# Kernel optimization log

Measured on AMD Instinct MI355X. Metric: run time of the kernel, lower is better.

The kernel has to match this reference:

```python
import jax, jax.numpy as jnp
import numpy as np

K = 3          # kernel_size
P = K // 2     # padding


def setup_inputs() -> dict:
    key = jax.random.key(0)
    # [B, C, H, W]; first C-4 channels are per-class probabilities, last 4 are box offsets
    points = jax.random.normal(key, (4, 84, 512, 512), dtype=jnp.float32)
    return {"points": points}


def reference(points):
    # Peak (point) NMS: keep a pixel iff torch.argmax over its KxK window of
    # max-class-probability lands exactly on the window center.
    # torch.argmax returns the FIRST flat index attaining the max, so the center
    # survives iff it is strictly greater than every earlier (row-major) window
    # element and >= every later element.
    probs = jnp.max(points[:, :-4], axis=1)            # [B, H, W]
    B, H, W = probs.shape
    padded = jnp.pad(probs, ((0, 0), (P, P), (P, P)))  # zero pad, matches F.pad default
    center_idx = P * K + P
    mask = jnp.ones((B, H, W), dtype=bool)
    for di in range(K):                                # small fixed K*K loop (8 iters)
        for dj in range(K):
            idx = di * K + dj
            if idx == center_idx:
                continue
            nb = padded[:, di:di + H, dj:dj + W]       # neighbor value at this offset
            cmp = (probs > nb) if idx < center_idx else (probs >= nb)
            mask = mask & cmp
    # non-peaks zeroed across ALL channels, exactly like the zeros_like + scatter
    return points * mask[:, None, :, :].astype(points.dtype)
```

## Files before the change

### kernel.cpp

```cpp
#include <hip/hip_runtime.h>

#define BB 4
#define CC 84
#define CM 80
#define HH 512
#define WW 512
#define HWSZ (HH * WW)
#define PG (HWSZ / 4)
#define NCH 4
#define CPC (CM / NCH)

typedef float v4f __attribute__((ext_vector_type(4)));

static __device__ __forceinline__ v4f vmax4(v4f a, v4f b) {
    v4f r;
    r.x = fmaxf(a.x, b.x);
    r.y = fmaxf(a.y, b.y);
    r.z = fmaxf(a.z, b.z);
    r.w = fmaxf(a.w, b.w);
    return r;
}

__global__ __launch_bounds__(256) void partial_max_kernel(const float* __restrict__ pts,
                                                          float* __restrict__ partial) {
    int tid = blockIdx.x * blockDim.x + threadIdx.x;
    int pg  = tid & (PG - 1);
    int r   = tid >> 16;
    int chunk = r % NCH;
    int b     = r / NCH;

    const v4f* base = (const v4f*)pts + ((size_t)b * CC + chunk * CPC) * PG + pg;
    v4f m = __builtin_nontemporal_load(base);
#pragma unroll 5
    for (int c = 1; c < CPC; ++c) {
        v4f v = __builtin_nontemporal_load(base + (size_t)c * PG);
        m = vmax4(m, v);
    }
    ((v4f*)partial)[((size_t)chunk * BB + b) * PG + pg] = m;
}

__global__ __launch_bounds__(256) void fused_mask_kernel(const float* __restrict__ partial,
                                                         float* __restrict__ mask) {
    int tid = blockIdx.x * blockDim.x + threadIdx.x;
    int pg  = tid & (PG - 1);
    int b   = tid >> 16;
    int off = pg << 2;
    int h   = off >> 9;
    int w0  = off & (WW - 1);

    float rows[3][6];
#pragma unroll
    for (int r = 0; r < 3; ++r) {
        int hh = h + r - 1;
        bool hv = (hh >= 0) & (hh < HH);
#pragma unroll
        for (int ci = 0; ci < 6; ++ci) {
            int ww = w0 + ci - 1;
            bool wv = (ww >= 0) & (ww < WW);
            float v = 0.0f;
            if (hv & wv) {
                int pidx = hh * WW + ww;
                v = partial[(size_t)(0 * BB + b) * HWSZ + pidx];
#pragma unroll
                for (int ch = 1; ch < NCH; ++ch)
                    v = fmaxf(v, partial[(size_t)(ch * BB + b) * HWSZ + pidx]);
            }
            rows[r][ci] = v;
        }
    }

    v4f fm;
#pragma unroll
    for (int j = 0; j < 4; ++j) {
        float v = rows[1][j + 1];
        bool m = (v >  rows[0][j]) & (v >  rows[0][j + 1]) & (v >  rows[0][j + 2])
               & (v >  rows[1][j]) & (v >= rows[1][j + 2])
               & (v >= rows[2][j]) & (v >= rows[2][j + 1]) & (v >= rows[2][j + 2]);
        float f = m ? 1.0f : 0.0f;
        if (j == 0) fm.x = f;
        else if (j == 1) fm.y = f;
        else if (j == 2) fm.z = f;
        else fm.w = f;
    }
    ((v4f*)mask)[(size_t)b * PG + pg] = fm;
}

__global__ __launch_bounds__(256) void mul_kernel(const float* __restrict__ pts,
                                                  const float* __restrict__ mask,
                                                  float* __restrict__ out) {
    int gid = blockIdx.x;
    int c   = gid % CC;
    int pc  = gid / CC;
    int b   = pc >> 8;
    int pg  = ((pc & 255) << 8) + threadIdx.x;

    v4f m = ((const v4f*)mask)[(size_t)b * PG + pg];
    size_t idx = ((size_t)b * CC + c) * PG + pg;

    unsigned nz = (__float_as_uint(m.x) | __float_as_uint(m.y) |
                   __float_as_uint(m.z) | __float_as_uint(m.w));
    v4f o;
    if (nz) {
        v4f v = __builtin_nontemporal_load((const v4f*)pts + idx);
        o.x = v.x * m.x;
        o.y = v.y * m.y;
        o.z = v.z * m.z;
        o.w = v.w * m.w;
    } else {
        o.x = 0.f; o.y = 0.f; o.z = 0.f; o.w = 0.f;
    }
    __builtin_nontemporal_store(o, (v4f*)out + idx);
}

__global__ __launch_bounds__(256) void probs_kernel_fb(const float* __restrict__ pts,
                                                       float* __restrict__ probs) {
    int tid = blockIdx.x * blockDim.x + threadIdx.x;
    int pix = tid << 2;
    int b   = pix >> 18;
    int off = pix & (HWSZ - 1);
    const float4* base = (const float4*)(pts + (size_t)b * CC * HWSZ + off);
    float4 m = base[0];
#pragma unroll 4
    for (int c = 1; c < CM; ++c) {
        float4 v = base[c * (HWSZ / 4)];
        m.x = fmaxf(m.x, v.x); m.y = fmaxf(m.y, v.y);
        m.z = fmaxf(m.z, v.z); m.w = fmaxf(m.w, v.w);
    }
    ((float4*)probs)[tid] = m;
}

__global__ __launch_bounds__(256) void nms_mul_kernel_fb(const float* __restrict__ pts,
                                                         const float* __restrict__ probs,
                                                         float* __restrict__ out) {
    int tid = blockIdx.x * blockDim.x + threadIdx.x;
    int pix = tid << 2;
    int b   = pix >> 18;
    int off = pix & (HWSZ - 1);
    int h   = off >> 9;
    int w0  = off & (WW - 1);
    const float* pb = probs + b * HWSZ;
    float rows[3][6];
#pragma unroll
    for (int r = 0; r < 3; ++r) {
        int hh = h + r - 1;
        bool hv = (hh >= 0) & (hh < HH);
        const float* rp = pb + hh * WW;
#pragma unroll
        for (int ci = 0; ci < 6; ++ci) {
            int ww = w0 + ci - 1;
            bool wv = (ww >= 0) & (ww < WW);
            rows[r][ci] = (hv & wv) ? rp[ww] : 0.0f;
        }
    }
    float fm[4];
    bool any = false;
#pragma unroll
    for (int j = 0; j < 4; ++j) {
        float v = rows[1][j + 1];
        bool m = (v >  rows[0][j]) & (v >  rows[0][j + 1]) & (v >  rows[0][j + 2])
               & (v >  rows[1][j]) & (v >= rows[1][j + 2])
               & (v >= rows[2][j]) & (v >= rows[2][j + 1]) & (v >= rows[2][j + 2]);
        fm[j] = m ? 1.0f : 0.0f;
        any |= m;
    }
    size_t bo = (size_t)b * CC * HWSZ + off;
    const float4* src = (const float4*)(pts + bo);
    float4* dst = (float4*)(out + bo);
    if (any) {
#pragma unroll 4
        for (int c = 0; c < CC; ++c) {
            float4 v = src[c * (HWSZ / 4)];
            float4 o;
            o.x = v.x * fm[0]; o.y = v.y * fm[1];
            o.z = v.z * fm[2]; o.w = v.w * fm[3];
            dst[c * (HWSZ / 4)] = o;
        }
    } else {
        float4 z = make_float4(0.f, 0.f, 0.f, 0.f);
#pragma unroll 4
        for (int c = 0; c < CC; ++c) dst[c * (HWSZ / 4)] = z;
    }
}

extern "C" void kernel_launch(void* const* d_in, const int* in_sizes, int n_in,
                              void* d_out, int out_size, void* d_ws, size_t ws_size,
                              hipStream_t stream) {
    const float* pts = (const float*)d_in[0];
    float* out = (float*)d_out;
    float* ws  = (float*)d_ws;

    const size_t MB4 = (size_t)BB * HWSZ * sizeof(float);
    dim3 blk(256);
    dim3 grd_pg(BB * PG / 256);

    if (ws_size >= (NCH + 1) * MB4) {
        float* partial = ws;
        float* mask    = ws + (size_t)NCH * BB * HWSZ;
        partial_max_kernel<<<dim3(BB * NCH * PG / 256), blk, 0, stream>>>(pts, partial);
        fused_mask_kernel<<<grd_pg, blk, 0, stream>>>(partial, mask);
        mul_kernel<<<dim3(BB * CC * (PG / 256)), blk, 0, stream>>>(pts, mask, out);
    } else {
        float* probs = ws;
        probs_kernel_fb<<<grd_pg, blk, 0, stream>>>(pts, probs);
        nms_mul_kernel_fb<<<grd_pg, blk, 0, stream>>>(pts, probs, out);
    }
}
```

Before: 613.8 us.

## Fuse max, mask and multiply stages into one cooperative grid-synced kernel

Replaces the three-launch pipeline with a single cooperative kernel that runs channel-max, 3x3 peak mask and masked multiply as grid-stride phases separated by grid syncs. The channel max is split into two 40-channel chunks instead of four, shrinking the partial buffer, and the multiply phase processes 42 channels per thread. First-pass loads are made regular (cacheable) rather than nontemporal, possibly letting the large last-level cache serve part of the second read of the input. Risks are grid-sync cost, lower memory-level parallelism per phase, and launch failure falling back to the old path.

```diff
diff --git a/kernel.cpp b/kernel.cpp
--- a/kernel.cpp
+++ b/kernel.cpp
@@ -1,4 +1,7 @@
 #include <hip/hip_runtime.h>
+#include <hip/hip_cooperative_groups.h>
+
+namespace cg = cooperative_groups;
 
 #define BB 4
 #define CC 84
@@ -7,8 +10,6 @@
 #define WW 512
 #define HWSZ (HH * WW)
 #define PG (HWSZ / 4)
-#define NCH 4
-#define CPC (CM / NCH)
 
 typedef float v4f __attribute__((ext_vector_type(4)));
 
@@ -21,6 +22,102 @@
     return r;
 }
 
+__global__ __launch_bounds__(256, 8) void fused_coop(const float* __restrict__ pts,
+                                                     float* __restrict__ wsp,
+                                                     float* __restrict__ out) {
+    float* partial = wsp;
+    float* mask    = wsp + (size_t)2 * BB * HWSZ;
+    const int nth  = gridDim.x * 256;
+    const int tid0 = blockIdx.x * 256 + threadIdx.x;
+
+    for (int t = tid0; t < BB * 2 * PG; t += nth) {
+        int pg    = t & (PG - 1);
+        int r     = t >> 16;
+        int b     = r & 3;
+        int chunk = r >> 2;
+        const v4f* base = (const v4f*)pts + ((size_t)b * CC + chunk * 40) * PG + pg;
+        v4f m = base[0];
+#pragma unroll 8
+        for (int c = 1; c < 40; ++c)
+            m = vmax4(m, base[(size_t)c * PG]);
+        ((v4f*)partial)[((size_t)chunk * BB + b) * PG + pg] = m;
+    }
+    cg::this_grid().sync();
+
+    for (int t = tid0; t < BB * PG; t += nth) {
+        int pg  = t & (PG - 1);
+        int b   = t >> 16;
+        int off = pg << 2;
+        int h   = off >> 9;
+        int w0  = off & (WW - 1);
+
+        const float* p0 = partial + (size_t)b * HWSZ;
+        const float* p1 = partial + (size_t)(BB + b) * HWSZ;
+
+        float rows[3][6];
+#pragma unroll
+        for (int rr = 0; rr < 3; ++rr) {
+            int hh = h + rr - 1;
+            bool hv = (hh >= 0) & (hh < HH);
+#pragma unroll
+            for (int ci = 0; ci < 6; ++ci) {
+                int ww = w0 + ci - 1;
+                bool wv = (ww >= 0) & (ww < WW);
+                float v = 0.0f;
+                if (hv & wv) {
+                    int pidx = hh * WW + ww;
+                    v = fmaxf(p0[pidx], p1[pidx]);
+                }
+                rows[rr][ci] = v;
+            }
+        }
+
+        v4f fm;
+#pragma unroll
+        for (int j = 0; j < 4; ++j) {
+            float v = rows[1][j + 1];
+            bool m = (v >  rows[0][j]) & (v >  rows[0][j + 1]) & (v >  rows[0][j + 2])
+                   & (v >  rows[1][j]) & (v >= rows[1][j + 2])
+                   & (v >= rows[2][j]) & (v >= rows[2][j + 1]) & (v >= rows[2][j + 2]);
+            float f = m ? 1.0f : 0.0f;
+            if (j == 0) fm.x = f;
+            else if (j == 1) fm.y = f;
+            else if (j == 2) fm.z = f;
+            else fm.w = f;
+        }
+        ((v4f*)mask)[(size_t)b * PG + pg] = fm;
+    }
+    cg::this_grid().sync();
+
+    for (int t = tid0; t < BB * 2 * PG; t += nth) {
+        int pg   = t & (PG - 1);
+        int r    = t >> 16;
+        int b    = r >> 1;
+        int half = r & 1;
+        v4f m = ((const v4f*)mask)[(size_t)b * PG + pg];
+        unsigned nz = (__float_as_uint(m.x) | __float_as_uint(m.y) |
+                       __float_as_uint(m.z) | __float_as_uint(m.w));
+        size_t base = ((size_t)b * CC + half * 42) * PG + pg;
+        if (nz) {
+#pragma unroll 7
+            for (int j = 0; j < 42; ++j) {
+                v4f v = __builtin_nontemporal_load((const v4f*)pts + base + (size_t)j * PG);
+                v4f o = v * m;
+                __builtin_nontemporal_store(o, (v4f*)out + base + (size_t)j * PG);
+            }
+        } else {
+            v4f z;
+            z.x = 0.f; z.y = 0.f; z.z = 0.f; z.w = 0.f;
+#pragma unroll 7
+            for (int j = 0; j < 42; ++j)
+                __builtin_nontemporal_store(z, (v4f*)out + base + (size_t)j * PG);
+        }
+    }
+}
+
+#define NCH 4
+#define CPC (CM / NCH)
+
 __global__ __launch_bounds__(256) void partial_max_kernel(const float* __restrict__ pts,
                                                           float* __restrict__ partial) {
     int tid = blockIdx.x * blockDim.x + threadIdx.x;
@@ -28,14 +125,11 @@
     int r   = tid >> 16;
     int chunk = r % NCH;
     int b     = r / NCH;
-
     const v4f* base = (const v4f*)pts + ((size_t)b * CC + chunk * CPC) * PG + pg;
-    v4f m = __builtin_nontemporal_load(base);
+    v4f m = base[0];
 #pragma unroll 5
-    for (int c = 1; c < CPC; ++c) {
-        v4f v = __builtin_nontemporal_load(base + (size_t)c * PG);
-        m = vmax4(m, v);
-    }
+    for (int c = 1; c < CPC; ++c)
+        m = vmax4(m, base[(size_t)c * PG]);
     ((v4f*)partial)[((size_t)chunk * BB + b) * PG + pg] = m;
 }
 
@@ -60,7 +154,7 @@
             float v = 0.0f;
             if (hv & wv) {
                 int pidx = hh * WW + ww;
-                v = partial[(size_t)(0 * BB + b) * HWSZ + pidx];
+                v = partial[(size_t)b * HWSZ + pidx];
 #pragma unroll
                 for (int ch = 1; ch < NCH; ++ch)
                     v = fmaxf(v, partial[(size_t)(ch * BB + b) * HWSZ + pidx]);
@@ -96,90 +190,16 @@
 
     v4f m = ((const v4f*)mask)[(size_t)b * PG + pg];
     size_t idx = ((size_t)b * CC + c) * PG + pg;
-
     unsigned nz = (__float_as_uint(m.x) | __float_as_uint(m.y) |
                    __float_as_uint(m.z) | __float_as_uint(m.w));
     v4f o;
     if (nz) {
         v4f v = __builtin_nontemporal_load((const v4f*)pts + idx);
-        o.x = v.x * m.x;
-        o.y = v.y * m.y;
-        o.z = v.z * m.z;
-        o.w = v.w * m.w;
+        o.x = v.x * m.x; o.y = v.y * m.y; o.z = v.z * m.z; o.w = v.w * m.w;
     } else {
         o.x = 0.f; o.y = 0.f; o.z = 0.f; o.w = 0.f;
     }
     __builtin_nontemporal_store(o, (v4f*)out + idx);
-}
-
-__global__ __launch_bounds__(256) void probs_kernel_fb(const float* __restrict__ pts,
-                                                       float* __restrict__ probs) {
-    int tid = blockIdx.x * blockDim.x + threadIdx.x;
-    int pix = tid << 2;
-    int b   = pix >> 18;
-    int off = pix & (HWSZ - 1);
-    const float4* base = (const float4*)(pts + (size_t)b * CC * HWSZ + off);
-    float4 m = base[0];
-#pragma unroll 4
-    for (int c = 1; c < CM; ++c) {
-        float4 v = base[c * (HWSZ / 4)];
-        m.x = fmaxf(m.x, v.x); m.y = fmaxf(m.y, v.y);
-        m.z = fmaxf(m.z, v.z); m.w = fmaxf(m.w, v.w);
-    }
-    ((float4*)probs)[tid] = m;
-}
-
-__global__ __launch_bounds__(256) void nms_mul_kernel_fb(const float* __restrict__ pts,
-                                                         const float* __restrict__ probs,
-                                                         float* __restrict__ out) {
-    int tid = blockIdx.x * blockDim.x + threadIdx.x;
-    int pix = tid << 2;
-    int b   = pix >> 18;
-    int off = pix & (HWSZ - 1);
-    int h   = off >> 9;
-    int w0  = off & (WW - 1);
-    const float* pb = probs + b * HWSZ;
-    float rows[3][6];
-#pragma unroll
-    for (int r = 0; r < 3; ++r) {
-        int hh = h + r - 1;
-        bool hv = (hh >= 0) & (hh < HH);
-        const float* rp = pb + hh * WW;
-#pragma unroll
-        for (int ci = 0; ci < 6; ++ci) {
-            int ww = w0 + ci - 1;
-            bool wv = (ww >= 0) & (ww < WW);
-            rows[r][ci] = (hv & wv) ? rp[ww] : 0.0f;
-        }
-    }
-    float fm[4];
-    bool any = false;
-#pragma unroll
-    for (int j = 0; j < 4; ++j) {
-        float v = rows[1][j + 1];
-        bool m = (v >  rows[0][j]) & (v >  rows[0][j + 1]) & (v >  rows[0][j + 2])
-               & (v >  rows[1][j]) & (v >= rows[1][j + 2])
-               & (v >= rows[2][j]) & (v >= rows[2][j + 1]) & (v >= rows[2][j + 2]);
-        fm[j] = m ? 1.0f : 0.0f;
-        any |= m;
-    }
-    size_t bo = (size_t)b * CC * HWSZ + off;
-    const float4* src = (const float4*)(pts + bo);
-    float4* dst = (float4*)(out + bo);
-    if (any) {
-#pragma unroll 4
-        for (int c = 0; c < CC; ++c) {
-            float4 v = src[c * (HWSZ / 4)];
-            float4 o;
-            o.x = v.x * fm[0]; o.y = v.y * fm[1];
-            o.z = v.z * fm[2]; o.w = v.w * fm[3];
-            dst[c * (HWSZ / 4)] = o;
-        }
-    } else {
-        float4 z = make_float4(0.f, 0.f, 0.f, 0.f);
-#pragma unroll 4
-        for (int c = 0; c < CC; ++c) dst[c * (HWSZ / 4)] = z;
-    }
 }
 
 extern "C" void kernel_launch(void* const* d_in, const int* in_sizes, int n_in,
@@ -190,18 +210,27 @@
     float* ws  = (float*)d_ws;
 
     const size_t MB4 = (size_t)BB * HWSZ * sizeof(float);
+
+    if (ws_size >= 3 * MB4) {
+        void* args[] = {(void*)&pts, (void*)&ws, (void*)&out};
+        hipError_t e = hipLaunchCooperativeKernel((const void*)fused_coop,
+                                                  dim3(2048), dim3(256),
+                                                  args, 0, stream);
+        if (e != hipSuccess) {
+            (void)hipGetLastError();
+            e = hipLaunchCooperativeKernel((const void*)fused_coop,
+                                           dim3(1024), dim3(256),
+                                           args, 0, stream);
+        }
+        if (e == hipSuccess) return;
+        (void)hipGetLastError();
+    }
+
     dim3 blk(256);
     dim3 grd_pg(BB * PG / 256);
-
-    if (ws_size >= (NCH + 1) * MB4) {
-        float* partial = ws;
-        float* mask    = ws + (size_t)NCH * BB * HWSZ;
-        partial_max_kernel<<<dim3(BB * NCH * PG / 256), blk, 0, stream>>>(pts, partial);
-        fused_mask_kernel<<<grd_pg, blk, 0, stream>>>(partial, mask);
-        mul_kernel<<<dim3(BB * CC * (PG / 256)), blk, 0, stream>>>(pts, mask, out);
-    } else {
-        float* probs = ws;
-        probs_kernel_fb<<<grd_pg, blk, 0, stream>>>(pts, probs);
-        nms_mul_kernel_fb<<<grd_pg, blk, 0, stream>>>(pts, probs, out);
-    }
-}
+    float* partial = ws;
+    float* maskp   = ws + (size_t)NCH * BB * HWSZ;
+    partial_max_kernel<<<dim3(BB * NCH * PG / 256), blk, 0, stream>>>(pts, partial);
+    fused_mask_kernel<<<grd_pg, blk, 0, stream>>>(partial, maskp);
+    mul_kernel<<<dim3(BB * CC * (PG / 256)), blk, 0, stream>>>(pts, maskp, out);
+}
```

Result: slower. 1.245 ms (+102.9%).
